# Kernel optimization log

Hardware: AMD Instinct MI355X
Metric: run time of the kernel (lower is better)

Reference implementation:

```python
import math
import jax, jax.numpy as jnp
import numpy as np
from jax import lax

MUL = 16           # multiplicity of 0e and 1o in input and output irreps
NRB = 8            # num_radial_basis
DIAMETER = 3.0
STEPS = (1.0, 1.0, 1.0)
DIM = 4 * MUL      # 16 scalars + 16 vectors * 3 = 64 channels


def _constants():
    # lattice from __init__: arange(-s, s+1) * step per axis, s = floor(r/step)
    r = DIAMETER / 2
    axes = [np.arange(-math.floor(r / st), math.floor(r / st) + 1.0) * st for st in STEPS]
    lattice = np.stack(np.meshgrid(*axes, indexing='ij'), axis=-1)  # [Kx,Ky,Kz,3]
    d = np.linalg.norm(lattice, axis=-1)                            # [Kx,Ky,Kz]
    # soft_one_hot_linspace(basis='smooth_finite', cutoff=True)
    values = np.linspace(0.0, r, NRB + 2)[1:-1]
    step = values[1] - values[0]
    diff = (d[..., None] - values) / step
    inside = diff ** 2 < 1.0
    emb = np.where(inside, 1.14136 * np.exp(2.0) * np.exp(-2.0 / np.where(inside, 1.0 - diff ** 2, 1.0)), 0.0)
    # spherical harmonics, normalize=True, normalization='component'
    n = lattice / np.maximum(d[..., None], 1e-12)  # unit vectors; 0 at the origin voxel
    sh0 = np.ones_like(d)                          # Y_0 (component normalized)
    sh1 = np.sqrt(3.0) * n                         # Y_1 (component normalized)
    return emb.astype(np.float32), sh0.astype(np.float32), sh1.astype(np.float32)

EMB, SH0, SH1 = _constants()
KX, KY, KZ = SH0.shape  # 3,3,3


def setup_inputs() -> dict:
    key = jax.random.key(0)
    ks = jax.random.split(key, 7)
    B, G = 4, 32
    return {
        'x': jax.random.normal(ks[0], (B, G, G, G, DIM), jnp.float32),
        'W_sc0': jax.random.normal(ks[1], (MUL, MUL), jnp.float32),  # Linear 0e->0e
        'W_sc1': jax.random.normal(ks[2], (MUL, MUL), jnp.float32),  # Linear 1o->1o
        'w1': jax.random.normal(ks[3], (NRB, MUL, MUL), jnp.float32),  # path 0e x 0e -> 0e
        'w2': jax.random.normal(ks[4], (NRB, MUL, MUL), jnp.float32),  # path 0e x 1o -> 1o
        'w3': jax.random.normal(ks[5], (NRB, MUL, MUL), jnp.float32),  # path 1o x 0e -> 1o
        'w4': jax.random.normal(ks[6], (NRB, MUL, MUL), jnp.float32),  # path 1o x 1o -> 0e
    }


def _kernel(w1, w2, w3, w4):
    # radial basis -> per-voxel path weights, divided by kernel volume (as in source)
    emb, sh0, sh1 = jnp.asarray(EMB), jnp.asarray(SH0), jnp.asarray(SH1)
    norm = float(KX * KY * KZ)
    W1, W2, W3, W4 = [jnp.einsum('xyzk,kio->xyzio', emb, w) / norm for w in (w1, w2, w3, w4)]
    # path normalization: each output irrep receives 2 paths of fan_in mul*1 = 16 -> 1/sqrt(32)
    alpha = 1.0 / np.sqrt(2.0 * MUL)
    # tp.right blocks (Clebsch-Gordan contractions, lmax=1):
    k00 = alpha * W1 * sh0[..., None, None]                                              # [.,i,o]
    k01 = alpha * jnp.einsum('xyzio,xyzm->xyziom', W2, sh1).reshape(KX, KY, KZ, MUL, 3 * MUL)
    k10 = (alpha / np.sqrt(3.0)) * jnp.einsum('xyzio,xyzm->xyzimo', W4, sh1).reshape(KX, KY, KZ, 3 * MUL, MUL)
    k11 = alpha * jnp.einsum('xyzio,mn->xyzimon', W3 * sh0[..., None, None],
                             jnp.eye(3, dtype=W3.dtype)).reshape(KX, KY, KZ, 3 * MUL, 3 * MUL)
    return jnp.concatenate([jnp.concatenate([k00, k01], axis=-1),
                            jnp.concatenate([k10, k11], axis=-1)], axis=-2)  # [Kx,Ky,Kz,64,64]


def reference(x, W_sc0, W_sc1, w1, w2, w3, w4):
    B, X, Y, Z, _ = x.shape
    inv_sqrt_mul = 1.0 / np.sqrt(MUL)
    # self-connection: e3nn Linear per irrep (applied pointwise over b,x,y,z)
    xs = x[..., :MUL]                                   # [B,X,Y,Z,16] scalars
    xv = x[..., MUL:].reshape(B, X, Y, Z, MUL, 3)       # [B,X,Y,Z,16,3] vectors
    sc_s = (xs @ W_sc0) * inv_sqrt_mul
    sc_v = jnp.einsum('bxyzic,io->bxyzoc', xv, W_sc1) * inv_sqrt_mul
    sc = jnp.concatenate([sc_s, sc_v.reshape(B, X, Y, Z, 3 * MUL)], axis=-1)
    # position-dependent equivariant kernel + standard 3D conv
    k = _kernel(w1, w2, w3, w4)
    conv = lax.conv_general_dilated(x, k, (1, 1, 1), 'SAME',
                                    dimension_numbers=('NXYZC', 'XYZIO', 'NXYZC'))
    return sc + conv
```

## Files before the change

### kernel.cpp

```cpp
#include <hip/hip_runtime.h>

typedef unsigned short u16;
typedef unsigned int u32;
typedef __bf16 bf16x8 __attribute__((ext_vector_type(8)));
typedef float f32x4 __attribute__((ext_vector_type(4)));
typedef u32 u32x4 __attribute__((ext_vector_type(4)));

#define AS1 __attribute__((address_space(1)))
#define AS3 __attribute__((address_space(3)))

__device__ __align__(16) u16 g_kT[27 * 64 * 64];
__device__ __align__(16) u16 g_kTr[27 * 8 * 512];

__device__ __forceinline__ u16 f2bf(float f) {
    unsigned int u = __float_as_uint(f);
    u += 0x7FFFu + ((u >> 16) & 1u);
    return (u16)(u >> 16);
}

__device__ __forceinline__ u32 pack_bf(float a, float b) {
    u32 ua = __float_as_uint(a) + 0x8000u;
    u32 ub = __float_as_uint(b) + 0x8000u;
    return __builtin_amdgcn_perm(ub, ua, 0x07060302u);
}

__global__ __launch_bounds__(64) void build_k(
    const float* __restrict__ Wsc0, const float* __restrict__ Wsc1,
    const float* __restrict__ w1, const float* __restrict__ w2,
    const float* __restrict__ w3, const float* __restrict__ w4)
{
    const int t = blockIdx.x;
    const int c = threadIdx.x;
    const int dx = t / 9 - 1, dy = (t / 3) % 3 - 1, dz = t % 3 - 1;
    const float d = sqrtf((float)(dx * dx + dy * dy + dz * dz));
    const float step = 1.5f / 9.0f;
    float emb[8];
#pragma unroll
    for (int k = 0; k < 8; ++k) {
        float diff = (d - (float)(k + 1) * step) / step;
        float q = diff * diff;
        emb[k] = (q < 1.0f) ? 1.14136f * expf(2.0f - 2.0f / (1.0f - q)) : 0.0f;
    }
    const float dn = fmaxf(d, 1e-12f);
    const float s3 = 1.7320508075688772f;
    const float sh1[3] = { s3 * (float)dx / dn, s3 * (float)dy / dn, s3 * (float)dz / dn };
    const float alpha  = 0.17677669529663687f;
    const float alpha3 = alpha * 0.57735026918962576f;

    u16* outp = &g_kT[(t * 64 + c) * 64];
    const int base2 = ((t * 2 + (c >> 5)) * 2 + ((c >> 4) & 1)) * 2;
    const int l15c  = c & 15;
    auto put = [&](int r, float v) {
        u16 h = f2bf(v);
        outp[r] = h;
        g_kTr[(base2 + (r >> 5)) * 512 + (((r >> 3) & 3) * 16 + l15c) * 8 + (r & 7)] = h;
    };

    if (c < 16) {
        const int o = c;
#pragma unroll
        for (int i = 0; i < 16; ++i) {
            float W1 = 0.f, W4 = 0.f;
#pragma unroll
            for (int k = 0; k < 8; ++k) {
                W1 += emb[k] * w1[k * 256 + i * 16 + o];
                W4 += emb[k] * w4[k * 256 + i * 16 + o];
            }
            W1 *= (1.0f / 27.0f); W4 *= (1.0f / 27.0f);
            float v0 = alpha * W1;
            if (t == 13) v0 += 0.25f * Wsc0[i * 16 + o];
            put(i, v0);
            const float base = alpha3 * W4;
#pragma unroll
            for (int m = 0; m < 3; ++m) put(16 + 3 * i + m, base * sh1[m]);
        }
    } else {
        const int o = (c - 16) / 3, nc = (c - 16) % 3;
#pragma unroll
        for (int i = 0; i < 16; ++i) {
            float W2 = 0.f, W3 = 0.f;
#pragma unroll
            for (int k = 0; k < 8; ++k) {
                W2 += emb[k] * w2[k * 256 + i * 16 + o];
                W3 += emb[k] * w3[k * 256 + i * 16 + o];
            }
            W2 *= (1.0f / 27.0f); W3 *= (1.0f / 27.0f);
            put(i, alpha * W2 * sh1[nc]);
#pragma unroll
            for (int m = 0; m < 3; ++m) {
                float v = (m == nc) ? alpha * W3 : 0.0f;
                if (t == 13 && m == nc) v += 0.25f * Wsc1[i * 16 + o];
                put(16 + 3 * i + m, v);
            }
        }
    }
}

__global__ __launch_bounds__(256) void cvt_x(
    const float* __restrict__ x, u16* __restrict__ xb, u32* __restrict__ zp)
{
    const int tid = threadIdx.x;
    if (blockIdx.x == 0) {
        u32x4 z = {0u, 0u, 0u, 0u};
        *reinterpret_cast<u32x4*>(zp + tid * 4) = z;
    }
    const size_t base = ((size_t)blockIdx.x * 256 + tid) * 8;
    const float4* s = reinterpret_cast<const float4*>(x + base);
    float4 v0 = s[0], v1 = s[1];
    u32x4 p;
    p[0] = pack_bf(v0.x, v0.y); p[1] = pack_bf(v0.z, v0.w);
    p[2] = pack_bf(v1.x, v1.y); p[3] = pack_bf(v1.z, v1.w);
    *reinterpret_cast<u32x4*>(xb + base) = p;
}

#define NROWS5 1020
#define NCHUNK5 128
#define LDSB   (NCHUNK5 * 1024)

#define ISSUE_B(s, t) \
  { const char* _p = bTr + (t) * 8192; \
    asm volatile("global_load_dwordx4 %0, %4, off\n\t" \
                 "global_load_dwordx4 %1, %4, off offset:1024\n\t" \
                 "global_load_dwordx4 %2, %4, off offset:2048\n\t" \
                 "global_load_dwordx4 %3, %4, off offset:3072" \
                 : "=&v"(B##s##0), "=&v"(B##s##1), "=&v"(B##s##2), "=&v"(B##s##3) \
                 : "v"(_p)); }

#define LOADA2(s, i0, i1, RCC) { \
  const int _r  = rbase + (RCC); \
  const int _o0 = _r * 128 + ((kg ^ (_r & 7)) << 4); \
  A##s##_##i0 = *reinterpret_cast<const bf16x8*>(abase + _o0); \
  A##s##_##i1 = *reinterpret_cast<const bf16x8*>(abase + (_o0 ^ 64)); }

#define RCC5(T, YY, MT) ((((T)/9)*340 + ((((T)/3)%3) + (YY))*34 + ((T)%3) + (MT)*16))

#define LOAD_A16(s, T) \
  LOADA2(s, 0,  1,  RCC5(T,0,0)) \
  LOADA2(s, 2,  3,  RCC5(T,0,1)) \
  LOADA2(s, 4,  5,  RCC5(T,1,0)) \
  LOADA2(s, 6,  7,  RCC5(T,1,1)) \
  LOADA2(s, 8,  9,  RCC5(T,2,0)) \
  LOADA2(s, 10, 11, RCC5(T,2,1)) \
  LOADA2(s, 12, 13, RCC5(T,3,0)) \
  LOADA2(s, 14, 15, RCC5(T,3,1))

#define WAITV(N) \
  asm volatile("s_waitcnt vmcnt(" #N ")" ::: "memory"); \
  __builtin_amdgcn_sched_barrier(0);

#define BC(x) __builtin_bit_cast(bf16x8, x)
#define MF(b_, a_, c_) __builtin_amdgcn_mfma_f32_16x16x32_bf16(BC(b_), a_, c_, 0, 0, 0)

#define MFMA32(bs, as) \
  acc000 = MF(B##bs##0, A##as##_0,  acc000);  acc001 = MF(B##bs##2, A##as##_0,  acc001); \
  acc010 = MF(B##bs##0, A##as##_2,  acc010);  acc011 = MF(B##bs##2, A##as##_2,  acc011); \
  acc100 = MF(B##bs##0, A##as##_4,  acc100);  acc101 = MF(B##bs##2, A##as##_4,  acc101); \
  acc110 = MF(B##bs##0, A##as##_6,  acc110);  acc111 = MF(B##bs##2, A##as##_6,  acc111); \
  acc200 = MF(B##bs##0, A##as##_8,  acc200);  acc201 = MF(B##bs##2, A##as##_8,  acc201); \
  acc210 = MF(B##bs##0, A##as##_10, acc210);  acc211 = MF(B##bs##2, A##as##_10, acc211); \
  acc300 = MF(B##bs##0, A##as##_12, acc300);  acc301 = MF(B##bs##2, A##as##_12, acc301); \
  acc310 = MF(B##bs##0, A##as##_14, acc310);  acc311 = MF(B##bs##2, A##as##_14, acc311); \
  acc000 = MF(B##bs##1, A##as##_1,  acc000);  acc001 = MF(B##bs##3, A##as##_1,  acc001); \
  acc010 = MF(B##bs##1, A##as##_3,  acc010);  acc011 = MF(B##bs##3, A##as##_3,  acc011); \
  acc100 = MF(B##bs##1, A##as##_5,  acc100);  acc101 = MF(B##bs##3, A##as##_5,  acc101); \
  acc110 = MF(B##bs##1, A##as##_7,  acc110);  acc111 = MF(B##bs##3, A##as##_7,  acc111); \
  acc200 = MF(B##bs##1, A##as##_9,  acc200);  acc201 = MF(B##bs##3, A##as##_9,  acc201); \
  acc210 = MF(B##bs##1, A##as##_11, acc210);  acc211 = MF(B##bs##3, A##as##_11, acc211); \
  acc300 = MF(B##bs##1, A##as##_13, acc300);  acc301 = MF(B##bs##3, A##as##_13, acc301); \
  acc310 = MF(B##bs##1, A##as##_15, acc310);  acc311 = MF(B##bs##3, A##as##_15, acc311);

__global__ __launch_bounds__(256, 1) void conv_mfma5(
    const u16* __restrict__ xb, const u32* __restrict__ zp,
    float* __restrict__ out)
{
    extern __shared__ u16 xt[];

    const int bid0 = blockIdx.x;
    const int bid  = (bid0 & 7) * 64 + (bid0 >> 3);
    const int b    = bid >> 7;
    const int X    = (bid >> 2) & 31;
    const int y0   = (bid & 3) << 3;
    const int tid  = threadIdx.x;
    const int wv   = tid >> 6;
    const int lane = tid & 63;
    const int l15  = lane & 15;
    const int kg   = lane >> 4;
    const int yh   = wv >> 1;
    const int nh   = wv & 1;

    const char* bTr = (const char*)g_kTr + nh * 4096 + lane * 16;

    u32x4 B00, B01, B02, B03, B10, B11, B12, B13, B20, B21, B22, B23;
    bf16x8 A0_0, A0_1, A0_2,  A0_3,  A0_4,  A0_5,  A0_6,  A0_7,
           A0_8, A0_9, A0_10, A0_11, A0_12, A0_13, A0_14, A0_15;
    bf16x8 A1_0, A1_1, A1_2,  A1_3,  A1_4,  A1_5,  A1_6,  A1_7,
           A1_8, A1_9, A1_10, A1_11, A1_12, A1_13, A1_14, A1_15;

    ISSUE_B(0, 1)
    ISSUE_B(1, 3)

    {
        const int rloc = lane >> 3;
        const int swz  = (lane & 7) ^ rloc;
#pragma unroll
        for (int i = 0; i < 32; ++i) {
            const int c = wv * 32 + i;
            const int row = c * 8 + rloc;
            const int dxx = row / 340;
            const int rem = row - dxx * 340;
            const int yi  = rem / 34;
            const int zid = rem - yi * 34;
            const int xin = X + dxx - 1;
            const int yin = y0 + yi - 1;
            const int zin = zid - 1;
            const bool inb = (row < NROWS5) & ((unsigned)xin < 32u)
                           & ((unsigned)yin < 32u) & ((unsigned)zin < 32u);
            const u16* src = inb
                ? xb + ((size_t)(((b * 32 + xin) * 32 + yin) * 32 + zin) * 64 + swz * 8)
                : (const u16*)zp;
            __builtin_amdgcn_global_load_lds((const AS1 u32*)src,
                                             (AS3 u32*)&xt[c * 512], 16, 0, 0);
        }
    }
    asm volatile("s_waitcnt vmcnt(0)" ::: "memory");
    __syncthreads();

    const char* abase = reinterpret_cast<const char*>(xt);
    const int rbase = yh * 136 + l15;

    const f32x4 z4 = {0.f, 0.f, 0.f, 0.f};
    f32x4 acc000 = z4, acc001 = z4, acc010 = z4, acc011 = z4;
    f32x4 acc100 = z4, acc101 = z4, acc110 = z4, acc111 = z4;
    f32x4 acc200 = z4, acc201 = z4, acc210 = z4, acc211 = z4;
    f32x4 acc300 = z4, acc301 = z4, acc310 = z4, acc311 = z4;

    LOAD_A16(0, 1)

    ISSUE_B(2, 4)   LOAD_A16(1, 3)   WAITV(8)  MFMA32(0, 0)
    ISSUE_B(0, 5)   LOAD_A16(0, 4)   WAITV(8)  MFMA32(1, 1)
    ISSUE_B(1, 7)   LOAD_A16(1, 5)   WAITV(8)  MFMA32(2, 0)
    ISSUE_B(2, 9)   LOAD_A16(0, 7)   WAITV(8)  MFMA32(0, 1)
    ISSUE_B(0, 10)  LOAD_A16(1, 9)   WAITV(8)  MFMA32(1, 0)
    ISSUE_B(1, 11)  LOAD_A16(0, 10)  WAITV(8)  MFMA32(2, 1)
    ISSUE_B(2, 12)  LOAD_A16(1, 11)  WAITV(8)  MFMA32(0, 0)
    ISSUE_B(0, 13)  LOAD_A16(0, 12)  WAITV(8)  MFMA32(1, 1)
    ISSUE_B(1, 14)  LOAD_A16(1, 13)  WAITV(8)  MFMA32(2, 0)
    ISSUE_B(2, 15)  LOAD_A16(0, 14)  WAITV(8)  MFMA32(0, 1)
    ISSUE_B(0, 16)  LOAD_A16(1, 15)  WAITV(8)  MFMA32(1, 0)
    ISSUE_B(1, 17)  LOAD_A16(0, 16)  WAITV(8)  MFMA32(2, 1)
    ISSUE_B(2, 19)  LOAD_A16(1, 17)  WAITV(8)  MFMA32(0, 0)
    ISSUE_B(0, 21)  LOAD_A16(0, 19)  WAITV(8)  MFMA32(1, 1)
    ISSUE_B(1, 22)  LOAD_A16(1, 21)  WAITV(8)  MFMA32(2, 0)
    ISSUE_B(2, 23)  LOAD_A16(0, 22)  WAITV(8)  MFMA32(0, 1)
    ISSUE_B(0, 25)  LOAD_A16(1, 23)  WAITV(8)  MFMA32(1, 0)
                    LOAD_A16(0, 25)  WAITV(4)  MFMA32(2, 1)
                                     WAITV(0)  MFMA32(0, 0)

    float* obase = out + (((size_t)(b * 32 + X) * 32 + (y0 + yh * 4)) * 32) * 64
                 + nh * 32 + kg * 4;
    *reinterpret_cast<f32x4*>(obase + l15 * 64)                    = acc000;
    *reinterpret_cast<f32x4*>(obase + l15 * 64 + 16)               = acc001;
    *reinterpret_cast<f32x4*>(obase + (16 + l15) * 64)             = acc010;
    *reinterpret_cast<f32x4*>(obase + (16 + l15) * 64 + 16)        = acc011;
    *reinterpret_cast<f32x4*>(obase + 2048 + l15 * 64)             = acc100;
    *reinterpret_cast<f32x4*>(obase + 2048 + l15 * 64 + 16)        = acc101;
    *reinterpret_cast<f32x4*>(obase + 2048 + (16 + l15) * 64)      = acc110;
    *reinterpret_cast<f32x4*>(obase + 2048 + (16 + l15) * 64 + 16) = acc111;
    *reinterpret_cast<f32x4*>(obase + 4096 + l15 * 64)             = acc200;
    *reinterpret_cast<f32x4*>(obase + 4096 + l15 * 64 + 16)        = acc201;
    *reinterpret_cast<f32x4*>(obase + 4096 + (16 + l15) * 64)      = acc210;
    *reinterpret_cast<f32x4*>(obase + 4096 + (16 + l15) * 64 + 16) = acc211;
    *reinterpret_cast<f32x4*>(obase + 6144 + l15 * 64)             = acc300;
    *reinterpret_cast<f32x4*>(obase + 6144 + l15 * 64 + 16)        = acc301;
    *reinterpret_cast<f32x4*>(obase + 6144 + (16 + l15) * 64)      = acc310;
    *reinterpret_cast<f32x4*>(obase + 6144 + (16 + l15) * 64 + 16) = acc311;
}

#define ZS 68
#define NROWS 408

__global__ __launch_bounds__(256, 2) void conv_mfma_fb(
    const float* __restrict__ x, float* __restrict__ out)
{
    __shared__ __align__(16) u16 xts[NROWS * ZS];
    const int bid0 = blockIdx.x;
    const int bid  = (bid0 & 7) * 256 + (bid0 >> 3);
    const int b   = bid >> 9;
    const int X   = (bid >> 4) & 31;
    const int y0  = (bid & 15) << 1;
    const int tid = threadIdx.x;

    {
        const int pr = tid >> 2;
        const int q  = tid & 3;
#pragma unroll
        for (int pass = 0; pass < 7; ++pass) {
            const int idx = pass * 64 + pr;
            if (idx < NROWS) {
                const int rid = idx / 34;
                const int zid = idx - rid * 34;
                const int xin = X + (rid >> 2) - 1;
                const int yin = y0 + (rid & 3) - 1;
                const int zin = zid - 1;
                u32x4 p0 = {0u,0u,0u,0u}, p1 = {0u,0u,0u,0u};
                if ((unsigned)xin < 32u && (unsigned)yin < 32u && (unsigned)zin < 32u) {
                    const float4* src = reinterpret_cast<const float4*>(
                        x + ((((b * 32 + xin) * 32 + yin) * 32 + zin) * 64 + q * 16));
                    float4 v0 = src[0], v1 = src[1], v2 = src[2], v3 = src[3];
                    p0[0] = pack_bf(v0.x, v0.y); p0[1] = pack_bf(v0.z, v0.w);
                    p0[2] = pack_bf(v1.x, v1.y); p0[3] = pack_bf(v1.z, v1.w);
                    p1[0] = pack_bf(v2.x, v2.y); p1[1] = pack_bf(v2.z, v2.w);
                    p1[2] = pack_bf(v3.x, v3.y); p1[3] = pack_bf(v3.z, v3.w);
                }
                u16* dst = &xts[idx * ZS + q * 16];
                *reinterpret_cast<u32x4*>(dst)     = p0;
                *reinterpret_cast<u32x4*>(dst + 8) = p1;
            }
        }
    }
    __syncthreads();

    const int w    = tid >> 6;
    const int lane = tid & 63;
    const int l15  = lane & 15;
    const int kg   = lane >> 4;
    const int mh   = w >> 1;
    const int nh   = w & 1;
    const int chb  = kg * 8;

    const u16* abase = &xts[l15 * ZS + chb];
    const u16* bbase = &g_kT[(nh * 32 + l15) * 64 + chb];

    const f32x4 z4 = {0.f, 0.f, 0.f, 0.f};
    f32x4 acc[2][2] = {{z4, z4}, {z4, z4}};

    constexpr int NT = 19;
    constexpr int TAPS[NT] = {1,3,4,5,7,9,10,11,12,13,14,15,16,17,19,21,22,23,25};

#pragma unroll
    for (int ti = 0; ti < NT; ++ti) {
        const int t = TAPS[ti];
        const int dxt = t / 9, dyt = (t / 3) % 3, dzt = t % 3;
        const int rid = dxt * 4 + mh + dyt;
        bf16x8 bfr[4], afr[4];
#pragma unroll
        for (int kb = 0; kb < 2; ++kb)
#pragma unroll
        for (int nt = 0; nt < 2; ++nt)
            bfr[kb*2+nt] = *reinterpret_cast<const bf16x8*>(
                bbase + (t * 64 + nt * 16) * 64 + kb * 32);
#pragma unroll
        for (int kb = 0; kb < 2; ++kb)
#pragma unroll
        for (int mt = 0; mt < 2; ++mt)
            afr[kb*2+mt] = *reinterpret_cast<const bf16x8*>(
                abase + (rid * 34 + dzt + mt * 16) * ZS + kb * 32);
#pragma unroll
        for (int kb = 0; kb < 2; ++kb)
#pragma unroll
        for (int mt = 0; mt < 2; ++mt)
#pragma unroll
        for (int nt = 0; nt < 2; ++nt)
            acc[mt][nt] = __builtin_amdgcn_mfma_f32_16x16x32_bf16(
                bfr[kb*2+nt], afr[kb*2+mt], acc[mt][nt], 0, 0, 0);
    }

    float* obase = out + (((b * 32 + X) * 32 + (y0 + mh)) * 32) * 64 + nh * 32 + kg * 4;
#pragma unroll
    for (int mt = 0; mt < 2; ++mt)
#pragma unroll
        for (int nt = 0; nt < 2; ++nt) {
            float4 v;
            v.x = acc[mt][nt][0]; v.y = acc[mt][nt][1];
            v.z = acc[mt][nt][2]; v.w = acc[mt][nt][3];
            *reinterpret_cast<float4*>(obase + (mt * 16 + l15) * 64 + nt * 16) = v;
        }
}

extern "C" void kernel_launch(void* const* d_in, const int* in_sizes, int n_in,
                              void* d_out, int out_size, void* d_ws, size_t ws_size,
                              hipStream_t stream)
{
    const float* x    = (const float*)d_in[0];
    const float* Wsc0 = (const float*)d_in[1];
    const float* Wsc1 = (const float*)d_in[2];
    const float* w1   = (const float*)d_in[3];
    const float* w2   = (const float*)d_in[4];
    const float* w3   = (const float*)d_in[5];
    const float* w4   = (const float*)d_in[6];
    float* out = (float*)d_out;

    build_k<<<dim3(27), dim3(64), 0, stream>>>(Wsc0, Wsc1, w1, w2, w3, w4);

    const size_t xb_bytes = (size_t)4 * 32 * 32 * 32 * 64 * 2;
    if (ws_size >= 4096 + xb_bytes) {
        u32* zp = (u32*)d_ws;
        u16* xb = (u16*)((char*)d_ws + 4096);
        cvt_x<<<dim3(4096), dim3(256), 0, stream>>>(x, xb, zp);
        conv_mfma5<<<dim3(512), dim3(256), LDSB, stream>>>(xb, zp, out);
    } else {
        conv_mfma_fb<<<dim3(2048), dim3(256), 0, stream>>>(x, out);
    }
}
```

Baseline: 57.25 us.

## Fuse prep kernels and split conv into 512-thread blocks with per-plane staged loads

Merges the kernel-weight build and the x-to-bf16 conversion into one launch, removing one kernel launch. The conv kernel moves to 512 threads per block, with each wave computing half as many output rows. The input halo is staged into LDS by x-plane, and a partial wait plus barrier lets MFMA work on the first tap planes start before all planes have arrived. LDS use grows with plane padding and the kernel relies on hand-placed waitcnt counts across more outstanding B buffers, which is fragile.

```diff
diff --git a/kernel.cpp b/kernel.cpp
--- a/kernel.cpp
+++ b/kernel.cpp
@@ -24,98 +24,98 @@
     return __builtin_amdgcn_perm(ub, ua, 0x07060302u);
 }
 
-__global__ __launch_bounds__(64) void build_k(
+__global__ __launch_bounds__(256) void prep(
     const float* __restrict__ Wsc0, const float* __restrict__ Wsc1,
     const float* __restrict__ w1, const float* __restrict__ w2,
-    const float* __restrict__ w3, const float* __restrict__ w4)
-{
-    const int t = blockIdx.x;
-    const int c = threadIdx.x;
-    const int dx = t / 9 - 1, dy = (t / 3) % 3 - 1, dz = t % 3 - 1;
-    const float d = sqrtf((float)(dx * dx + dy * dy + dz * dz));
-    const float step = 1.5f / 9.0f;
-    float emb[8];
-#pragma unroll
-    for (int k = 0; k < 8; ++k) {
-        float diff = (d - (float)(k + 1) * step) / step;
-        float q = diff * diff;
-        emb[k] = (q < 1.0f) ? 1.14136f * expf(2.0f - 2.0f / (1.0f - q)) : 0.0f;
-    }
-    const float dn = fmaxf(d, 1e-12f);
-    const float s3 = 1.7320508075688772f;
-    const float sh1[3] = { s3 * (float)dx / dn, s3 * (float)dy / dn, s3 * (float)dz / dn };
-    const float alpha  = 0.17677669529663687f;
-    const float alpha3 = alpha * 0.57735026918962576f;
-
-    u16* outp = &g_kT[(t * 64 + c) * 64];
-    const int base2 = ((t * 2 + (c >> 5)) * 2 + ((c >> 4) & 1)) * 2;
-    const int l15c  = c & 15;
-    auto put = [&](int r, float v) {
-        u16 h = f2bf(v);
-        outp[r] = h;
-        g_kTr[(base2 + (r >> 5)) * 512 + (((r >> 3) & 3) * 16 + l15c) * 8 + (r & 7)] = h;
-    };
-
-    if (c < 16) {
-        const int o = c;
-#pragma unroll
-        for (int i = 0; i < 16; ++i) {
-            float W1 = 0.f, W4 = 0.f;
-#pragma unroll
-            for (int k = 0; k < 8; ++k) {
-                W1 += emb[k] * w1[k * 256 + i * 16 + o];
-                W4 += emb[k] * w4[k * 256 + i * 16 + o];
-            }
-            W1 *= (1.0f / 27.0f); W4 *= (1.0f / 27.0f);
-            float v0 = alpha * W1;
-            if (t == 13) v0 += 0.25f * Wsc0[i * 16 + o];
-            put(i, v0);
-            const float base = alpha3 * W4;
-#pragma unroll
-            for (int m = 0; m < 3; ++m) put(16 + 3 * i + m, base * sh1[m]);
-        }
-    } else {
-        const int o = (c - 16) / 3, nc = (c - 16) % 3;
-#pragma unroll
-        for (int i = 0; i < 16; ++i) {
-            float W2 = 0.f, W3 = 0.f;
-#pragma unroll
-            for (int k = 0; k < 8; ++k) {
-                W2 += emb[k] * w2[k * 256 + i * 16 + o];
-                W3 += emb[k] * w3[k * 256 + i * 16 + o];
-            }
-            W2 *= (1.0f / 27.0f); W3 *= (1.0f / 27.0f);
-            put(i, alpha * W2 * sh1[nc]);
-#pragma unroll
-            for (int m = 0; m < 3; ++m) {
-                float v = (m == nc) ? alpha * W3 : 0.0f;
-                if (t == 13 && m == nc) v += 0.25f * Wsc1[i * 16 + o];
-                put(16 + 3 * i + m, v);
-            }
-        }
-    }
-}
-
-__global__ __launch_bounds__(256) void cvt_x(
+    const float* __restrict__ w3, const float* __restrict__ w4,
     const float* __restrict__ x, u16* __restrict__ xb, u32* __restrict__ zp)
 {
     const int tid = threadIdx.x;
-    if (blockIdx.x == 0) {
-        u32x4 z = {0u, 0u, 0u, 0u};
-        *reinterpret_cast<u32x4*>(zp + tid * 4) = z;
-    }
-    const size_t base = ((size_t)blockIdx.x * 256 + tid) * 8;
-    const float4* s = reinterpret_cast<const float4*>(x + base);
-    float4 v0 = s[0], v1 = s[1];
-    u32x4 p;
-    p[0] = pack_bf(v0.x, v0.y); p[1] = pack_bf(v0.z, v0.w);
-    p[2] = pack_bf(v1.x, v1.y); p[3] = pack_bf(v1.z, v1.w);
-    *reinterpret_cast<u32x4*>(xb + base) = p;
-}
-
-#define NROWS5 1020
-#define NCHUNK5 128
-#define LDSB   (NCHUNK5 * 1024)
+    if (blockIdx.x < 27) {
+        if (tid >= 64) return;
+        const int t = blockIdx.x;
+        const int c = tid;
+        const int dx = t / 9 - 1, dy = (t / 3) % 3 - 1, dz = t % 3 - 1;
+        const float d = sqrtf((float)(dx * dx + dy * dy + dz * dz));
+        const float step = 1.5f / 9.0f;
+        float emb[8];
+#pragma unroll
+        for (int k = 0; k < 8; ++k) {
+            float diff = (d - (float)(k + 1) * step) / step;
+            float q = diff * diff;
+            emb[k] = (q < 1.0f) ? 1.14136f * expf(2.0f - 2.0f / (1.0f - q)) : 0.0f;
+        }
+        const float dn = fmaxf(d, 1e-12f);
+        const float s3 = 1.7320508075688772f;
+        const float sh1[3] = { s3 * dx / dn, s3 * dy / dn, s3 * dz / dn };
+        const float alpha  = 0.17677669529663687f;
+        const float alpha3 = alpha * 0.57735026918962576f;
+
+        u16* outp = &g_kT[(t * 64 + c) * 64];
+        const int base2 = ((t * 2 + (c >> 5)) * 2 + ((c >> 4) & 1)) * 2;
+        const int l15c  = c & 15;
+        auto put = [&](int r, float v) {
+            u16 h = f2bf(v);
+            outp[r] = h;
+            g_kTr[(base2 + (r >> 5)) * 512 + (((r >> 3) & 3) * 16 + l15c) * 8 + (r & 7)] = h;
+        };
+
+        if (c < 16) {
+            const int o = c;
+#pragma unroll
+            for (int i = 0; i < 16; ++i) {
+                float W1 = 0.f, W4 = 0.f;
+#pragma unroll
+                for (int k = 0; k < 8; ++k) {
+                    W1 += emb[k] * w1[k * 256 + i * 16 + o];
+                    W4 += emb[k] * w4[k * 256 + i * 16 + o];
+                }
+                W1 *= (1.0f / 27.0f); W4 *= (1.0f / 27.0f);
+                float v0 = alpha * W1;
+                if (t == 13) v0 += 0.25f * Wsc0[i * 16 + o];
+                put(i, v0);
+                const float base = alpha3 * W4;
+#pragma unroll
+                for (int m = 0; m < 3; ++m) put(16 + 3 * i + m, base * sh1[m]);
+            }
+        } else {
+            const int o = (c - 16) / 3, nc = (c - 16) % 3;
+#pragma unroll
+            for (int i = 0; i < 16; ++i) {
+                float W2 = 0.f, W3 = 0.f;
+#pragma unroll
+                for (int k = 0; k < 8; ++k) {
+                    W2 += emb[k] * w2[k * 256 + i * 16 + o];
+                    W3 += emb[k] * w3[k * 256 + i * 16 + o];
+                }
+                W2 *= (1.0f / 27.0f); W3 *= (1.0f / 27.0f);
+                put(i, alpha * W2 * sh1[nc]);
+#pragma unroll
+                for (int m = 0; m < 3; ++m) {
+                    float v = (m == nc) ? alpha * W3 : 0.0f;
+                    if (t == 13 && m == nc) v += 0.25f * Wsc1[i * 16 + o];
+                    put(16 + 3 * i + m, v);
+                }
+            }
+        }
+    } else {
+        const int bid2 = blockIdx.x - 27;
+        if (bid2 == 0) {
+            u32x4 z = {0u, 0u, 0u, 0u};
+            *reinterpret_cast<u32x4*>(zp + tid * 4) = z;
+        }
+        const size_t base = ((size_t)bid2 * 256 + tid) * 8;
+        const float4* s = reinterpret_cast<const float4*>(x + base);
+        float4 v0 = s[0], v1 = s[1];
+        u32x4 p;
+        p[0] = pack_bf(v0.x, v0.y); p[1] = pack_bf(v0.z, v0.w);
+        p[2] = pack_bf(v1.x, v1.y); p[3] = pack_bf(v1.z, v1.w);
+        *reinterpret_cast<u32x4*>(xb + base) = p;
+    }
+}
+
+#define PLS 384
+#define LDSB (3 * 48 * 1024)
 
 #define ISSUE_B(s, t) \
   { const char* _p = bTr + (t) * 8192; \
@@ -132,44 +132,36 @@
   A##s##_##i0 = *reinterpret_cast<const bf16x8*>(abase + _o0); \
   A##s##_##i1 = *reinterpret_cast<const bf16x8*>(abase + (_o0 ^ 64)); }
 
-#define RCC5(T, YY, MT) ((((T)/9)*340 + ((((T)/3)%3) + (YY))*34 + ((T)%3) + (MT)*16))
-
-#define LOAD_A16(s, T) \
-  LOADA2(s, 0,  1,  RCC5(T,0,0)) \
-  LOADA2(s, 2,  3,  RCC5(T,0,1)) \
-  LOADA2(s, 4,  5,  RCC5(T,1,0)) \
-  LOADA2(s, 6,  7,  RCC5(T,1,1)) \
-  LOADA2(s, 8,  9,  RCC5(T,2,0)) \
-  LOADA2(s, 10, 11, RCC5(T,2,1)) \
-  LOADA2(s, 12, 13, RCC5(T,3,0)) \
-  LOADA2(s, 14, 15, RCC5(T,3,1))
+#define RCC6(T, YY, MT) (((T)/9)*PLS + ((((T)/3)%3) + (YY))*34 + ((T)%3) + (MT)*16)
+
+#define LOAD_A8(s, T) \
+  LOADA2(s, 0, 1, RCC6(T,0,0)) \
+  LOADA2(s, 2, 3, RCC6(T,0,1)) \
+  LOADA2(s, 4, 5, RCC6(T,1,0)) \
+  LOADA2(s, 6, 7, RCC6(T,1,1))
 
 #define WAITV(N) \
   asm volatile("s_waitcnt vmcnt(" #N ")" ::: "memory"); \
   __builtin_amdgcn_sched_barrier(0);
 
+#define BARRIER() \
+  asm volatile("s_barrier" ::: "memory"); \
+  __builtin_amdgcn_sched_barrier(0);
+
 #define BC(x) __builtin_bit_cast(bf16x8, x)
 #define MF(b_, a_, c_) __builtin_amdgcn_mfma_f32_16x16x32_bf16(BC(b_), a_, c_, 0, 0, 0)
 
-#define MFMA32(bs, as) \
-  acc000 = MF(B##bs##0, A##as##_0,  acc000);  acc001 = MF(B##bs##2, A##as##_0,  acc001); \
-  acc010 = MF(B##bs##0, A##as##_2,  acc010);  acc011 = MF(B##bs##2, A##as##_2,  acc011); \
-  acc100 = MF(B##bs##0, A##as##_4,  acc100);  acc101 = MF(B##bs##2, A##as##_4,  acc101); \
-  acc110 = MF(B##bs##0, A##as##_6,  acc110);  acc111 = MF(B##bs##2, A##as##_6,  acc111); \
-  acc200 = MF(B##bs##0, A##as##_8,  acc200);  acc201 = MF(B##bs##2, A##as##_8,  acc201); \
-  acc210 = MF(B##bs##0, A##as##_10, acc210);  acc211 = MF(B##bs##2, A##as##_10, acc211); \
-  acc300 = MF(B##bs##0, A##as##_12, acc300);  acc301 = MF(B##bs##2, A##as##_12, acc301); \
-  acc310 = MF(B##bs##0, A##as##_14, acc310);  acc311 = MF(B##bs##2, A##as##_14, acc311); \
-  acc000 = MF(B##bs##1, A##as##_1,  acc000);  acc001 = MF(B##bs##3, A##as##_1,  acc001); \
-  acc010 = MF(B##bs##1, A##as##_3,  acc010);  acc011 = MF(B##bs##3, A##as##_3,  acc011); \
-  acc100 = MF(B##bs##1, A##as##_5,  acc100);  acc101 = MF(B##bs##3, A##as##_5,  acc101); \
-  acc110 = MF(B##bs##1, A##as##_7,  acc110);  acc111 = MF(B##bs##3, A##as##_7,  acc111); \
-  acc200 = MF(B##bs##1, A##as##_9,  acc200);  acc201 = MF(B##bs##3, A##as##_9,  acc201); \
-  acc210 = MF(B##bs##1, A##as##_11, acc210);  acc211 = MF(B##bs##3, A##as##_11, acc211); \
-  acc300 = MF(B##bs##1, A##as##_13, acc300);  acc301 = MF(B##bs##3, A##as##_13, acc301); \
-  acc310 = MF(B##bs##1, A##as##_15, acc310);  acc311 = MF(B##bs##3, A##as##_15, acc311);
-
-__global__ __launch_bounds__(256, 1) void conv_mfma5(
+#define MFMA16(bs, as) \
+  acc000 = MF(B##bs##0, A##as##_0, acc000); acc001 = MF(B##bs##2, A##as##_0, acc001); \
+  acc010 = MF(B##bs##0, A##as##_2, acc010); acc011 = MF(B##bs##2, A##as##_2, acc011); \
+  acc100 = MF(B##bs##0, A##as##_4, acc100); acc101 = MF(B##bs##2, A##as##_4, acc101); \
+  acc110 = MF(B##bs##0, A##as##_6, acc110); acc111 = MF(B##bs##2, A##as##_6, acc111); \
+  acc000 = MF(B##bs##1, A##as##_1, acc000); acc001 = MF(B##bs##3, A##as##_1, acc001); \
+  acc010 = MF(B##bs##1, A##as##_3, acc010); acc011 = MF(B##bs##3, A##as##_3, acc011); \
+  acc100 = MF(B##bs##1, A##as##_5, acc100); acc101 = MF(B##bs##3, A##as##_5, acc101); \
+  acc110 = MF(B##bs##1, A##as##_7, acc110); acc111 = MF(B##bs##3, A##as##_7, acc111);
+
+__global__ __launch_bounds__(512, 2) void conv_mfma6(
     const u16* __restrict__ xb, const u32* __restrict__ zp,
     float* __restrict__ out)
 {
@@ -190,73 +182,80 @@
 
     const char* bTr = (const char*)g_kTr + nh * 4096 + lane * 16;
 
-    u32x4 B00, B01, B02, B03, B10, B11, B12, B13, B20, B21, B22, B23;
-    bf16x8 A0_0, A0_1, A0_2,  A0_3,  A0_4,  A0_5,  A0_6,  A0_7,
-           A0_8, A0_9, A0_10, A0_11, A0_12, A0_13, A0_14, A0_15;
-    bf16x8 A1_0, A1_1, A1_2,  A1_3,  A1_4,  A1_5,  A1_6,  A1_7,
-           A1_8, A1_9, A1_10, A1_11, A1_12, A1_13, A1_14, A1_15;
+    u32x4 B00, B01, B02, B03, B10, B11, B12, B13, B20, B21, B22, B23,
+          B30, B31, B32, B33, B40, B41, B42, B43;
+    bf16x8 A0_0, A0_1, A0_2, A0_3, A0_4, A0_5, A0_6, A0_7;
+    bf16x8 A1_0, A1_1, A1_2, A1_3, A1_4, A1_5, A1_6, A1_7;
 
     ISSUE_B(0, 1)
     ISSUE_B(1, 3)
+    ISSUE_B(2, 4)
+    ISSUE_B(3, 5)
+    ISSUE_B(4, 7)
 
     {
         const int rloc = lane >> 3;
         const int swz  = (lane & 7) ^ rloc;
 #pragma unroll
-        for (int i = 0; i < 32; ++i) {
-            const int c = wv * 32 + i;
-            const int row = c * 8 + rloc;
-            const int dxx = row / 340;
-            const int rem = row - dxx * 340;
-            const int yi  = rem / 34;
-            const int zid = rem - yi * 34;
-            const int xin = X + dxx - 1;
-            const int yin = y0 + yi - 1;
-            const int zin = zid - 1;
-            const bool inb = (row < NROWS5) & ((unsigned)xin < 32u)
-                           & ((unsigned)yin < 32u) & ((unsigned)zin < 32u);
-            const u16* src = inb
-                ? xb + ((size_t)(((b * 32 + xin) * 32 + yin) * 32 + zin) * 64 + swz * 8)
-                : (const u16*)zp;
-            __builtin_amdgcn_global_load_lds((const AS1 u32*)src,
-                                             (AS3 u32*)&xt[c * 512], 16, 0, 0);
-        }
-    }
-    asm volatile("s_waitcnt vmcnt(0)" ::: "memory");
-    __syncthreads();
+        for (int p = 0; p < 3; ++p) {
+#pragma unroll
+            for (int j = 0; j < 6; ++j) {
+                const int cip = wv * 6 + j;
+                const int c   = p * 48 + cip;
+                const int rip = cip * 8 + rloc;
+                const int yi  = rip / 34;
+                const int zid = rip - yi * 34;
+                const int xin = X + p - 1;
+                const int yin = y0 + yi - 1;
+                const int zin = zid - 1;
+                const bool inb = (rip < 340) & ((unsigned)xin < 32u)
+                               & ((unsigned)yin < 32u) & ((unsigned)zin < 32u);
+                const u16* src = inb
+                    ? xb + ((size_t)(((b * 32 + xin) * 32 + yin) * 32 + zin) * 64 + swz * 8)
+                    : (const u16*)zp;
+                __builtin_amdgcn_global_load_lds((const AS1 u32*)src,
+                                                 (AS3 u32*)&xt[c * 512], 16, 0, 0);
+            }
+        }
+    }
 
     const char* abase = reinterpret_cast<const char*>(xt);
-    const int rbase = yh * 136 + l15;
+    const int rbase = yh * 68 + l15;
 
     const f32x4 z4 = {0.f, 0.f, 0.f, 0.f};
     f32x4 acc000 = z4, acc001 = z4, acc010 = z4, acc011 = z4;
     f32x4 acc100 = z4, acc101 = z4, acc110 = z4, acc111 = z4;
-    f32x4 acc200 = z4, acc201 = z4, acc210 = z4, acc211 = z4;
-    f32x4 acc300 = z4, acc301 = z4, acc310 = z4, acc311 = z4;
-
-    LOAD_A16(0, 1)
-
-    ISSUE_B(2, 4)   LOAD_A16(1, 3)   WAITV(8)  MFMA32(0, 0)
-    ISSUE_B(0, 5)   LOAD_A16(0, 4)   WAITV(8)  MFMA32(1, 1)
-    ISSUE_B(1, 7)   LOAD_A16(1, 5)   WAITV(8)  MFMA32(2, 0)
-    ISSUE_B(2, 9)   LOAD_A16(0, 7)   WAITV(8)  MFMA32(0, 1)
-    ISSUE_B(0, 10)  LOAD_A16(1, 9)   WAITV(8)  MFMA32(1, 0)
-    ISSUE_B(1, 11)  LOAD_A16(0, 10)  WAITV(8)  MFMA32(2, 1)
-    ISSUE_B(2, 12)  LOAD_A16(1, 11)  WAITV(8)  MFMA32(0, 0)
-    ISSUE_B(0, 13)  LOAD_A16(0, 12)  WAITV(8)  MFMA32(1, 1)
-    ISSUE_B(1, 14)  LOAD_A16(1, 13)  WAITV(8)  MFMA32(2, 0)
-    ISSUE_B(2, 15)  LOAD_A16(0, 14)  WAITV(8)  MFMA32(0, 1)
-    ISSUE_B(0, 16)  LOAD_A16(1, 15)  WAITV(8)  MFMA32(1, 0)
-    ISSUE_B(1, 17)  LOAD_A16(0, 16)  WAITV(8)  MFMA32(2, 1)
-    ISSUE_B(2, 19)  LOAD_A16(1, 17)  WAITV(8)  MFMA32(0, 0)
-    ISSUE_B(0, 21)  LOAD_A16(0, 19)  WAITV(8)  MFMA32(1, 1)
-    ISSUE_B(1, 22)  LOAD_A16(1, 21)  WAITV(8)  MFMA32(2, 0)
-    ISSUE_B(2, 23)  LOAD_A16(0, 22)  WAITV(8)  MFMA32(0, 1)
-    ISSUE_B(0, 25)  LOAD_A16(1, 23)  WAITV(8)  MFMA32(1, 0)
-                    LOAD_A16(0, 25)  WAITV(4)  MFMA32(2, 1)
-                                     WAITV(0)  MFMA32(0, 0)
-
-    float* obase = out + (((size_t)(b * 32 + X) * 32 + (y0 + yh * 4)) * 32) * 64
+
+    WAITV(12)
+    BARRIER()
+    LOAD_A8(0, 1)
+    LOAD_A8(1, 3)   MFMA16(0, 0)
+    LOAD_A8(0, 4)   MFMA16(1, 1)
+    LOAD_A8(1, 5)   MFMA16(2, 0)
+    LOAD_A8(0, 7)   MFMA16(3, 1)
+                    MFMA16(4, 0)
+
+    ISSUE_B(0, 9)
+    ISSUE_B(1, 10)
+    WAITV(4)
+    BARRIER()
+    LOAD_A8(1, 9)
+    ISSUE_B(2, 11)  LOAD_A8(0, 10)            MFMA16(0, 1)
+    ISSUE_B(0, 12)  LOAD_A8(1, 11)  WAITV(8)  MFMA16(1, 0)
+    ISSUE_B(1, 13)  LOAD_A8(0, 12)  WAITV(8)  MFMA16(2, 1)
+    ISSUE_B(2, 14)  LOAD_A8(1, 13)  WAITV(8)  MFMA16(0, 0)
+    ISSUE_B(0, 15)  LOAD_A8(0, 14)  WAITV(8)  MFMA16(1, 1)
+    ISSUE_B(1, 16)  LOAD_A8(1, 15)  WAITV(8)  MFMA16(2, 0)
+    ISSUE_B(2, 17)  LOAD_A8(0, 16)  WAITV(8)  MFMA16(0, 1)
+    ISSUE_B(0, 19)  LOAD_A8(1, 17)  WAITV(8)  MFMA16(1, 0)
+    ISSUE_B(1, 21)  LOAD_A8(0, 19)  WAITV(8)  MFMA16(2, 1)
+    ISSUE_B(2, 22)  LOAD_A8(1, 21)  WAITV(8)  MFMA16(0, 0)
+    ISSUE_B(0, 23)  LOAD_A8(0, 22)  WAITV(8)  MFMA16(1, 1)
+    ISSUE_B(1, 25)  LOAD_A8(1, 23)  WAITV(8)  MFMA16(2, 0)
+                    LOAD_A8(0, 25)  WAITV(4)  MFMA16(0, 1)
+                                    WAITV(0)  MFMA16(1, 0)
+
+    float* obase = out + (((size_t)(b * 32 + X) * 32 + (y0 + yh * 2)) * 32) * 64
                  + nh * 32 + kg * 4;
     *reinterpret_cast<f32x4*>(obase + l15 * 64)                    = acc000;
     *reinterpret_cast<f32x4*>(obase + l15 * 64 + 16)               = acc001;
@@ -266,14 +265,6 @@
     *reinterpret_cast<f32x4*>(obase + 2048 + l15 * 64 + 16)        = acc101;
     *reinterpret_cast<f32x4*>(obase + 2048 + (16 + l15) * 64)      = acc110;
     *reinterpret_cast<f32x4*>(obase + 2048 + (16 + l15) * 64 + 16) = acc111;
-    *reinterpret_cast<f32x4*>(obase + 4096 + l15 * 64)             = acc200;
-    *reinterpret_cast<f32x4*>(obase + 4096 + l15 * 64 + 16)        = acc201;
-    *reinterpret_cast<f32x4*>(obase + 4096 + (16 + l15) * 64)      = acc210;
-    *reinterpret_cast<f32x4*>(obase + 4096 + (16 + l15) * 64 + 16) = acc211;
-    *reinterpret_cast<f32x4*>(obase + 6144 + l15 * 64)             = acc300;
-    *reinterpret_cast<f32x4*>(obase + 6144 + l15 * 64 + 16)        = acc301;
-    *reinterpret_cast<f32x4*>(obase + 6144 + (16 + l15) * 64)      = acc310;
-    *reinterpret_cast<f32x4*>(obase + 6144 + (16 + l15) * 64 + 16) = acc311;
 }
 
 #define ZS 68
@@ -390,15 +381,16 @@
     const float* w4   = (const float*)d_in[6];
     float* out = (float*)d_out;
 
-    build_k<<<dim3(27), dim3(64), 0, stream>>>(Wsc0, Wsc1, w1, w2, w3, w4);
-
     const size_t xb_bytes = (size_t)4 * 32 * 32 * 32 * 64 * 2;
     if (ws_size >= 4096 + xb_bytes) {
         u32* zp = (u32*)d_ws;
         u16* xb = (u16*)((char*)d_ws + 4096);
-        cvt_x<<<dim3(4096), dim3(256), 0, stream>>>(x, xb, zp);
-        conv_mfma5<<<dim3(512), dim3(256), LDSB, stream>>>(xb, zp, out);
+        prep<<<dim3(27 + 4096), dim3(256), 0, stream>>>(Wsc0, Wsc1, w1, w2, w3, w4,
+                                                        x, xb, zp);
+        conv_mfma6<<<dim3(512), dim3(512), LDSB, stream>>>(xb, zp, out);
     } else {
+        prep<<<dim3(27), dim3(256), 0, stream>>>(Wsc0, Wsc1, w1, w2, w3, w4,
+                                                 x, (u16*)nullptr, (u32*)nullptr);
         conv_mfma_fb<<<dim3(2048), dim3(256), 0, stream>>>(x, out);
     }
 }
```

Measured after the change: 53.79 us. -6.0%, faster.
